# Performance work log

Hardware: AMD Instinct MI355X
Metric: run time of the kernel (lower is better)

The kernel has to match this reference:

```python
import jax, jax.numpy as jnp
import numpy as np

B, L, D = 512, 33, 4096
P, K, H = 64, 512, 128  # proj_dim, topk, head hidden
LN_EPS = 1e-5


def setup_inputs() -> dict:
    key = jax.random.key(0)
    ks = jax.random.split(key, 12)
    s = lambda fan_in: 1.0 / np.sqrt(fan_in)
    return {
        "x": jax.random.normal(ks[0], (B, L, D), dtype=jnp.float32),
        "Wp": jax.random.uniform(ks[1], (P, L), jnp.float32, -s(L), s(L)),
        "bp": jax.random.uniform(ks[2], (P,), jnp.float32, -s(L), s(L)),
        "ws": jax.random.uniform(ks[3], (P,), jnp.float32, -s(P), s(P)),
        "bs": jax.random.uniform(ks[4], (), jnp.float32, -s(P), s(P)),
        "gamma": jnp.ones((P,), jnp.float32),
        "beta": jnp.zeros((P,), jnp.float32),
        "W1": jax.random.uniform(ks[5], (H, P), jnp.float32, -s(P), s(P)),
        "b1": jax.random.uniform(ks[6], (H,), jnp.float32, -s(P), s(P)),
        "W2": jax.random.uniform(ks[7], (2, H), jnp.float32, -s(H), s(H)),
        "b2": jax.random.uniform(ks[8], (2,), jnp.float32, -s(H), s(H)),
    }


def reference(x, Wp, bp, ws, bs, gamma, beta, W1, b1, W2, b2):
    # x: (B, L, D) -> per-dim layer trajectories projected to P
    h = jnp.einsum("bld,pl->bdp", x, Wp) + bp           # (B, D, P)
    scores = jnp.einsum("bdp,p->bd", h, ws) + bs         # (B, D)
    topk_scores, topk_idx = jax.lax.top_k(scores, K)     # (B, K)
    w = jax.nn.softmax(topk_scores, axis=-1)             # (B, K)
    topk_h = jnp.take_along_axis(h, topk_idx[:, :, None], axis=1)  # (B, K, P)
    out = jnp.einsum("bkp,bk->bp", topk_h, w)            # (B, P)
    # head: LayerNorm -> Linear -> GELU -> Linear (dropout in eval = identity)
    mu = jnp.mean(out, axis=-1, keepdims=True)
    var = jnp.mean((out - mu) ** 2, axis=-1, keepdims=True)
    z = (out - mu) * jax.lax.rsqrt(var + LN_EPS) * gamma + beta
    z = jax.nn.gelu(z @ W1.T + b1, approximate=False)
    return z @ W2.T + b2                                  # (B, 2)
```

## Files before the change

### kernel.cpp

```cpp
#include <hip/hip_runtime.h>
#include <math.h>

#define NB 512
#define LL 33
#define DD 4096
#define PP 64
#define KK 512
#define HH 128
#define LN_EPS 1e-5f
#define NT 512
#define NW (NT / 64)

__device__ __forceinline__ unsigned fkey(float s) {
    unsigned u = __float_as_uint(s);
    return (u & 0x80000000u) ? ~u : (u | 0x80000000u);
}

__device__ __forceinline__ float waveMax(float v) {
    #pragma unroll
    for (int o = 32; o > 0; o >>= 1) v = fmaxf(v, __shfl_xor(v, o));
    return v;
}
__device__ __forceinline__ float waveSum(float v) {
    #pragma unroll
    for (int o = 32; o > 0; o >>= 1) v += __shfl_xor(v, o);
    return v;
}

__global__ __launch_bounds__(NT) void sda_kernel(
    const float* __restrict__ x,
    const float* __restrict__ Wp, const float* __restrict__ bp,
    const float* __restrict__ ws, const float* __restrict__ bsp,
    const float* __restrict__ gamma, const float* __restrict__ beta,
    const float* __restrict__ W1, const float* __restrict__ b1,
    const float* __restrict__ W2, const float* __restrict__ b2,
    float* __restrict__ out)
{
    __shared__ __align__(16) float s_w[DD];
    __shared__ __align__(16) float s_xc[LL * 256];
    __shared__ float s_v[LL];
    __shared__ unsigned s_hist[NW][256];
    __shared__ unsigned s_scanA[256];
    __shared__ unsigned s_scanB[256];
    __shared__ float s_red[NW];
    __shared__ float s_y[LL];
    __shared__ float s_o[PP];
    __shared__ float s_g[HH];
    __shared__ float s_c, s_m, s_S;
    __shared__ unsigned s_prefix, s_kk, s_ceq;

    const int t = threadIdx.x;
    const int lane = t & 63;
    const int wv = t >> 6;
    const int b = blockIdx.x;
    const float* __restrict__ xb = x + (size_t)b * (LL * DD);

    if (t < LL) {
        float a = 0.f;
        for (int p = 0; p < PP; ++p) a += Wp[p * LL + t] * ws[p];
        s_v[t] = a;
    } else if (t == LL) {
        float a = bsp[0];
        for (int p = 0; p < PP; ++p) a += ws[p] * bp[p];
        s_c = a;
    }
    if (t == 0) { s_prefix = 0u; s_kk = KK; s_ceq = 0u; }
    __syncthreads();

    const float c0 = s_c;
    float4* s_w4 = (float4*)s_w;
    float4* s_xc4 = (float4*)s_xc;
    const float4* rp = (const float4*)xb;
    float4 cur0 = rp[t];
    float4 cur1 = rp[t + NT];
    float4 acc0 = make_float4(c0, c0, c0, c0);
    float4 acc1 = acc0;
    for (int l = 0; l < LL - 1; ++l) {
        const float4* np = rp + 1024;
        const float4 nxt0 = np[t];
        const float4 nxt1 = np[t + NT];
        const float vl = s_v[l];
        if (t < 64) s_xc4[l * 64 + t] = cur0;
        acc0.x += vl * cur0.x; acc0.y += vl * cur0.y; acc0.z += vl * cur0.z; acc0.w += vl * cur0.w;
        acc1.x += vl * cur1.x; acc1.y += vl * cur1.y; acc1.z += vl * cur1.z; acc1.w += vl * cur1.w;
        cur0 = nxt0; cur1 = nxt1; rp = np;
    }
    {
        const float vl = s_v[LL - 1];
        if (t < 64) s_xc4[(LL - 1) * 64 + t] = cur0;
        acc0.x += vl * cur0.x; acc0.y += vl * cur0.y; acc0.z += vl * cur0.z; acc0.w += vl * cur0.w;
        acc1.x += vl * cur1.x; acc1.y += vl * cur1.y; acc1.z += vl * cur1.z; acc1.w += vl * cur1.w;
    }

    unsigned ukey[8];
    s_w4[t] = acc0;
    s_w4[t + NT] = acc1;
    ukey[0] = fkey(acc0.x); ukey[1] = fkey(acc0.y); ukey[2] = fkey(acc0.z); ukey[3] = fkey(acc0.w);
    ukey[4] = fkey(acc1.x); ukey[5] = fkey(acc1.y); ukey[6] = fkey(acc1.z); ukey[7] = fkey(acc1.w);
    float lmax = fmaxf(fmaxf(fmaxf(acc0.x, acc0.y), fmaxf(acc0.z, acc0.w)),
                       fmaxf(fmaxf(acc1.x, acc1.y), fmaxf(acc1.z, acc1.w)));
    lmax = waveMax(lmax);
    if (lane == 0) s_red[wv] = lmax;
    __syncthreads();
    if (t == 0) {
        float m = s_red[0];
        for (int i = 1; i < NW; ++i) m = fmaxf(m, s_red[i]);
        s_m = m;
    }
    __syncthreads();

    for (int shift = 24; shift >= 0; shift -= 8) {
        for (int i = t; i < NW * 256; i += NT) ((unsigned*)s_hist)[i] = 0u;
        __syncthreads();
        const unsigned pfx = s_prefix;
        const unsigned hm = (shift == 24) ? 0u : (0xFFFFFFFFu << (shift + 8));
        #pragma unroll
        for (int i = 0; i < 8; ++i) {
            const unsigned u = ukey[i];
            if ((u & hm) == pfx)
                atomicAdd(&s_hist[wv][(u >> shift) & 255u], 1u);
        }
        __syncthreads();
        if (t < 256) {
            unsigned a = 0;
            for (int w = 0; w < NW; ++w) a += s_hist[w][t];
            s_scanA[t] = a;
        }
        __syncthreads();
        unsigned* src = s_scanA;
        unsigned* dst = s_scanB;
        for (int off = 1; off < 256; off <<= 1) {
            if (t < 256) dst[t] = src[t] + ((t + off < 256) ? src[t + off] : 0u);
            __syncthreads();
            unsigned* tmp = src; src = dst; dst = tmp;
        }
        if (t < 256) {
            const unsigned kk = s_kk;
            const unsigned mine = src[t];
            const unsigned above = (t == 255) ? 0u : src[t + 1];
            if (mine >= kk && above < kk) {
                s_prefix = pfx | ((unsigned)t << shift);
                s_kk = kk - above;
                s_ceq = mine - above;
            }
        }
        __syncthreads();
    }
    const unsigned T = s_prefix;
    const unsigned need_eq = s_kk;
    const unsigned count_eq = s_ceq;
    const float m = s_m;

    if (count_eq == need_eq) {
        float4 w0, w1;
        w0.x = (ukey[0] >= T) ? expf(acc0.x - m) : 0.f;
        w0.y = (ukey[1] >= T) ? expf(acc0.y - m) : 0.f;
        w0.z = (ukey[2] >= T) ? expf(acc0.z - m) : 0.f;
        w0.w = (ukey[3] >= T) ? expf(acc0.w - m) : 0.f;
        w1.x = (ukey[4] >= T) ? expf(acc1.x - m) : 0.f;
        w1.y = (ukey[5] >= T) ? expf(acc1.y - m) : 0.f;
        w1.z = (ukey[6] >= T) ? expf(acc1.z - m) : 0.f;
        w1.w = (ukey[7] >= T) ? expf(acc1.w - m) : 0.f;
        s_w4[t] = w0;
        s_w4[t + NT] = w1;
        float lsum = w0.x + w0.y + w0.z + w0.w + w1.x + w1.y + w1.z + w1.w;
        lsum = waveSum(lsum);
        if (lane == 0) s_red[wv] = lsum;
        __syncthreads();
        if (t == 0) {
            float S = 0.f;
            for (int i = 0; i < NW; ++i) S += s_red[i];
            s_S = S;
        }
        __syncthreads();
    } else {
        __syncthreads();
        if (t == 0) {
            unsigned taken = 0;
            float S = 0.f;
            for (int d = 0; d < DD; ++d) {
                const float s = s_w[d];
                const unsigned u = fkey(s);
                float w = 0.f;
                if (u > T) w = expf(s - m);
                else if (u == T && taken < need_eq) { w = expf(s - m); ++taken; }
                s_w[d] = w;
                S += w;
            }
            s_S = S;
        }
        __syncthreads();
    }
    const float invS = 1.0f / s_S;

    for (int k = 4; k >= 0; --k) {
        const int l = wv + NW * k;
        if (l < LL) {
            const float4* row = (const float4*)(xb + l * DD);
            float a = 0.f;
            #pragma unroll
            for (int j = 15; j >= 1; --j) {
                const int f = lane + j * 64;
                const float4 xv = row[f];
                const float4 w4 = s_w4[f];
                a += w4.x * xv.x + w4.y * xv.y + w4.z * xv.z + w4.w * xv.w;
            }
            {
                const float4 xv = s_xc4[l * 64 + lane];
                const float4 w4 = s_w4[lane];
                a += w4.x * xv.x + w4.y * xv.y + w4.z * xv.z + w4.w * xv.w;
            }
            a = waveSum(a);
            if (lane == 0) s_y[l] = a;
        }
    }
    __syncthreads();

    if (t < PP) {
        float a = 0.f;
        for (int l = 0; l < LL; ++l) a += Wp[t * LL + l] * s_y[l];
        s_o[t] = a * invS + bp[t];
    }
    __syncthreads();
    if (wv == 0) {
        const float o = s_o[lane];
        const float mu = waveSum(o) * (1.f / PP);
        const float dv = o - mu;
        const float var = waveSum(dv * dv) * (1.f / PP);
        s_o[lane] = dv * rsqrtf(var + LN_EPS) * gamma[lane] + beta[lane];
    }
    __syncthreads();
    if (t < HH) {
        float a = b1[t];
        for (int p = 0; p < PP; ++p) a += W1[t * PP + p] * s_o[p];
        s_g[t] = 0.5f * a * (1.f + erff(a * 0.70710678118654752440f));
    }
    __syncthreads();
    if (t < 2) {
        float a = b2[t];
        for (int j = 0; j < HH; ++j) a += W2[t * HH + j] * s_g[j];
        out[b * 2 + t] = a;
    }
}

extern "C" void kernel_launch(void* const* d_in, const int* in_sizes, int n_in,
                              void* d_out, int out_size, void* d_ws, size_t ws_size,
                              hipStream_t stream) {
    const float* x     = (const float*)d_in[0];
    const float* Wp    = (const float*)d_in[1];
    const float* bp    = (const float*)d_in[2];
    const float* ws    = (const float*)d_in[3];
    const float* bs    = (const float*)d_in[4];
    const float* gamma = (const float*)d_in[5];
    const float* beta  = (const float*)d_in[6];
    const float* W1    = (const float*)d_in[7];
    const float* b1    = (const float*)d_in[8];
    const float* W2    = (const float*)d_in[9];
    const float* b2    = (const float*)d_in[10];
    float* out = (float*)d_out;
    hipLaunchKernelGGL(sda_kernel, dim3(NB), dim3(NT), 0, stream,
                       x, Wp, bp, ws, bs, gamma, beta, W1, b1, W2, b2, out);
}
```

Measured before the change: 462.8 us.

## Deepen load prefetch, drop LDS row cache, use wave-shuffle scan for radix select

```diff
diff --git a/kernel.cpp b/kernel.cpp
--- a/kernel.cpp
+++ b/kernel.cpp
@@ -27,7 +27,7 @@
     return v;
 }
 
-__global__ __launch_bounds__(NT) void sda_kernel(
+__global__ __launch_bounds__(NT, 4) void sda_kernel(
     const float* __restrict__ x,
     const float* __restrict__ Wp, const float* __restrict__ bp,
     const float* __restrict__ ws, const float* __restrict__ bsp,
@@ -37,11 +37,8 @@
     float* __restrict__ out)
 {
     __shared__ __align__(16) float s_w[DD];
-    __shared__ __align__(16) float s_xc[LL * 256];
     __shared__ float s_v[LL];
     __shared__ unsigned s_hist[NW][256];
-    __shared__ unsigned s_scanA[256];
-    __shared__ unsigned s_scanB[256];
     __shared__ float s_red[NW];
     __shared__ float s_y[LL];
     __shared__ float s_o[PP];
@@ -69,27 +66,27 @@
 
     const float c0 = s_c;
     float4* s_w4 = (float4*)s_w;
-    float4* s_xc4 = (float4*)s_xc;
-    const float4* rp = (const float4*)xb;
-    float4 cur0 = rp[t];
-    float4 cur1 = rp[t + NT];
+    const float4* base = (const float4*)xb;
+    float4 pa[4], pb[4];
+    #pragma unroll
+    for (int s = 0; s < 4; ++s) {
+        pa[s] = base[s * 1024 + t];
+        pb[s] = base[s * 1024 + t + NT];
+    }
     float4 acc0 = make_float4(c0, c0, c0, c0);
     float4 acc1 = acc0;
-    for (int l = 0; l < LL - 1; ++l) {
-        const float4* np = rp + 1024;
-        const float4 nxt0 = np[t];
-        const float4 nxt1 = np[t + NT];
+    #pragma unroll
+    for (int l = 0; l < LL; ++l) {
+        const int s = l & 3;
+        const float4 xa = pa[s];
+        const float4 xc = pb[s];
+        if (l + 4 < LL) {
+            pa[s] = base[(l + 4) * 1024 + t];
+            pb[s] = base[(l + 4) * 1024 + t + NT];
+        }
         const float vl = s_v[l];
-        if (t < 64) s_xc4[l * 64 + t] = cur0;
-        acc0.x += vl * cur0.x; acc0.y += vl * cur0.y; acc0.z += vl * cur0.z; acc0.w += vl * cur0.w;
-        acc1.x += vl * cur1.x; acc1.y += vl * cur1.y; acc1.z += vl * cur1.z; acc1.w += vl * cur1.w;
-        cur0 = nxt0; cur1 = nxt1; rp = np;
-    }
-    {
-        const float vl = s_v[LL - 1];
-        if (t < 64) s_xc4[(LL - 1) * 64 + t] = cur0;
-        acc0.x += vl * cur0.x; acc0.y += vl * cur0.y; acc0.z += vl * cur0.z; acc0.w += vl * cur0.w;
-        acc1.x += vl * cur1.x; acc1.y += vl * cur1.y; acc1.z += vl * cur1.z; acc1.w += vl * cur1.w;
+        acc0.x += vl * xa.x; acc0.y += vl * xa.y; acc0.z += vl * xa.z; acc0.w += vl * xa.w;
+        acc1.x += vl * xc.x; acc1.y += vl * xc.y; acc1.z += vl * xc.z; acc1.w += vl * xc.w;
     }
 
     unsigned ukey[8];
@@ -121,27 +118,45 @@
                 atomicAdd(&s_hist[wv][(u >> shift) & 255u], 1u);
         }
         __syncthreads();
-        if (t < 256) {
-            unsigned a = 0;
-            for (int w = 0; w < NW; ++w) a += s_hist[w][t];
-            s_scanA[t] = a;
-        }
-        __syncthreads();
-        unsigned* src = s_scanA;
-        unsigned* dst = s_scanB;
-        for (int off = 1; off < 256; off <<= 1) {
-            if (t < 256) dst[t] = src[t] + ((t + off < 256) ? src[t + off] : 0u);
-            __syncthreads();
-            unsigned* tmp = src; src = dst; dst = tmp;
-        }
-        if (t < 256) {
+        if (t < 64) {
+            const int b4 = t * 4;
+            unsigned c0b = 0, c1b = 0, c2b = 0, c3b = 0;
+            for (int w = 0; w < NW; ++w) {
+                c0b += s_hist[w][b4 + 0];
+                c1b += s_hist[w][b4 + 1];
+                c2b += s_hist[w][b4 + 2];
+                c3b += s_hist[w][b4 + 3];
+            }
+            const unsigned s3 = c3b;
+            const unsigned s2 = c2b + s3;
+            const unsigned s1 = c1b + s2;
+            const unsigned s0 = c0b + s1;
+            unsigned inc = s0;
+            #pragma unroll
+            for (int off = 1; off < 64; off <<= 1) {
+                const int src = t + off;
+                const unsigned other = __shfl(inc, (src < 64) ? src : t);
+                inc += (src < 64) ? other : 0u;
+            }
+            const unsigned excl = inc - s0;
             const unsigned kk = s_kk;
-            const unsigned mine = src[t];
-            const unsigned above = (t == 255) ? 0u : src[t + 1];
-            if (mine >= kk && above < kk) {
-                s_prefix = pfx | ((unsigned)t << shift);
-                s_kk = kk - above;
-                s_ceq = mine - above;
+            const unsigned cm0 = excl + s0, cm1 = excl + s1,
+                           cm2 = excl + s2, cm3 = excl + s3;
+            if (cm0 >= kk && cm0 - c0b < kk) {
+                s_prefix = pfx | ((unsigned)(b4 + 0) << shift);
+                s_kk = kk - (cm0 - c0b); s_ceq = c0b;
+            }
+            if (cm1 >= kk && cm1 - c1b < kk) {
+                s_prefix = pfx | ((unsigned)(b4 + 1) << shift);
+                s_kk = kk - (cm1 - c1b); s_ceq = c1b;
+            }
+            if (cm2 >= kk && cm2 - c2b < kk) {
+                s_prefix = pfx | ((unsigned)(b4 + 2) << shift);
+                s_kk = kk - (cm2 - c2b); s_ceq = c2b;
+            }
+            if (cm3 >= kk && cm3 - c3b < kk) {
+                s_prefix = pfx | ((unsigned)(b4 + 3) << shift);
+                s_kk = kk - (cm3 - c3b); s_ceq = c3b;
             }
         }
         __syncthreads();
@@ -199,15 +214,10 @@
             const float4* row = (const float4*)(xb + l * DD);
             float a = 0.f;
             #pragma unroll
-            for (int j = 15; j >= 1; --j) {
+            for (int j = 15; j >= 0; --j) {
                 const int f = lane + j * 64;
                 const float4 xv = row[f];
                 const float4 w4 = s_w4[f];
-                a += w4.x * xv.x + w4.y * xv.y + w4.z * xv.z + w4.w * xv.w;
-            }
-            {
-                const float4 xv = s_xc4[l * 64 + lane];
-                const float4 w4 = s_w4[lane];
                 a += w4.x * xv.x + w4.y * xv.y + w4.z * xv.z + w4.w * xv.w;
             }
             a = waveSum(a);
```

Result: faster. 414.1 us (-10.5%).
